# Performance work log

Hardware: AMD Instinct MI355X
Metric: run time of the kernel (lower is better)

The kernel has to match this reference:

```python
import jax, jax.numpy as jnp
import numpy as np

N_NODES = 50000
N_EDGES = 300000
N_CLUSTERS = 100
IN_C = 256
OUT_C = 256


def setup_inputs() -> dict:
    key = jax.random.key(0)
    k1, k2, k3, k4, k5, k6 = jax.random.split(key, 6)
    X = jax.random.normal(k1, (N_NODES, IN_C), dtype=jnp.float32)
    # Cluster-GCN style block partition: contiguous clusters of equal size
    assign = ((jnp.arange(N_NODES) * N_CLUSTERS) // N_NODES).astype(jnp.int32)
    bs = N_NODES // N_CLUSTERS  # block (cluster) size
    src = jax.random.randint(k2, (N_EDGES,), 0, N_NODES)
    intra_dst = (src // bs) * bs + jax.random.randint(k3, (N_EDGES,), 0, bs)
    rand_dst = jax.random.randint(k4, (N_EDGES,), 0, N_NODES)
    dst = jnp.where(jax.random.uniform(k5, (N_EDGES,)) < 0.9, intra_dst, rand_dst)
    full_ei = jnp.stack([src, dst]).astype(jnp.int32)
    W = (jax.random.normal(k6, (IN_C, OUT_C), dtype=jnp.float32) / np.sqrt(IN_C)).astype(jnp.float32)
    b = jnp.zeros((OUT_C,), dtype=jnp.float32)
    return {"X": X, "W": W, "b": b, "assign": assign, "full_ei": full_ei}


def reference(X, W, b, assign, full_ei):
    # Equivalent to the per-cluster loop: GCNConv (add_self_loops=True, symmetric
    # normalization) applied to the subgraph of intra-cluster edges; clusters
    # with zero internal edges are skipped (nodes keep original features).
    N = X.shape[0]
    src, dst = full_ei[0], full_ei[1]
    intra = (assign[src] == assign[dst]).astype(X.dtype)  # [E]
    # per-cluster-subgraph degree, including self loop
    deg = jnp.ones((N,), X.dtype).at[dst].add(intra)  # [N]
    dis = jax.lax.rsqrt(deg)
    xW = X @ W  # [N, out_c]
    w_e = intra * dis[src] * dis[dst]  # [E]
    agg = jax.ops.segment_sum(w_e[:, None] * xW[src], dst, num_segments=N)
    agg = agg + xW / deg[:, None]  # self-loop term: norm = 1/deg
    out = agg + b
    has_edge = jax.ops.segment_sum(intra, assign[src], num_segments=N_CLUSTERS) > 0
    return jnp.where(has_edge[assign][:, None], out, X)
```

## Files before the change

kernel.cpp:

```cpp
#include <hip/hip_runtime.h>
#include <hip/hip_bf16.h>

#define N_NODES 50000
#define N_EDGES 300000
#define N_CLUSTERS 100
#define CH 256
#define CAP 32

typedef __attribute__((ext_vector_type(8))) short short8;
typedef __attribute__((ext_vector_type(4))) float f32x4;

static __device__ inline unsigned short f2bf(float f) {
    unsigned int u = __float_as_uint(f);
    u += 0x7fffu + ((u >> 16) & 1u);
    return (unsigned short)(u >> 16);
}


__global__ void init_kernel(int* __restrict__ indeg, int* __restrict__ flags) {
    int i = blockIdx.x * blockDim.x + threadIdx.x;
    if (i < N_NODES) indeg[i] = 0;
    if (i < N_CLUSTERS) flags[i] = 0;
}

__global__ void scatter_kernel(const int* __restrict__ ei, const int* __restrict__ assign,
                               int* __restrict__ indeg, int* __restrict__ flags,
                               int* __restrict__ csr) {
    int e = blockIdx.x * blockDim.x + threadIdx.x;
    if (e >= N_EDGES) return;
    int s = ei[e], d = ei[N_EDGES + e];
    int cs = assign[s];
    if (cs == assign[d]) {
        int p = atomicAdd(&indeg[d], 1);
        if (p < CAP) csr[d * CAP + p] = s;
        flags[cs] = 1;
    }
}

__global__ void convw_kernel(const float* __restrict__ W, unsigned short* __restrict__ Wt) {
    int n = blockIdx.x, k = threadIdx.x;
    Wt[n * CH + k] = f2bf(W[k * CH + n]);
}


#define BM 64
#define ALDS 264

__global__ __launch_bounds__(256, 2) void gemm_bf16(const float* __restrict__ X,
                                                    const unsigned short* __restrict__ Wt,
                                                    unsigned short* __restrict__ xWb) {
    __shared__ unsigned short Xs[BM * ALDS];
    int tid = threadIdx.x;
    int row0 = blockIdx.x * BM;
    int wid = tid >> 6, lane = tid & 63;
    int wn = wid * 64;
    int l15 = lane & 15, quad = lane >> 4;

    short8 breg[4][8];
#pragma unroll
    for (int ni = 0; ni < 4; ++ni) {
        const unsigned short* p = Wt + (size_t)(wn + ni * 16 + l15) * CH + quad * 8;
#pragma unroll
        for (int c = 0; c < 8; ++c)
            breg[ni][c] = *reinterpret_cast<const short8*>(p + c * 32);
    }

    int srow = tid >> 2;
    int scol = (tid & 3) * 64;
    int garow = row0 + srow; if (garow >= N_NODES) garow = N_NODES - 1;
    const float* gA = X + (size_t)garow * CH + scol;
    unsigned short* lA = &Xs[srow * ALDS + scol];
#pragma unroll
    for (int j = 0; j < 16; j += 2) {
        float4 u = *reinterpret_cast<const float4*>(gA + j * 4);
        float4 v = *reinterpret_cast<const float4*>(gA + j * 4 + 4);
        ushort4 lo = { f2bf(u.x), f2bf(u.y), f2bf(u.z), f2bf(u.w) };
        ushort4 hi = { f2bf(v.x), f2bf(v.y), f2bf(v.z), f2bf(v.w) };
        uint4 packed;
        packed.x = (unsigned)lo.x | ((unsigned)lo.y << 16);
        packed.y = (unsigned)lo.z | ((unsigned)lo.w << 16);
        packed.z = (unsigned)hi.x | ((unsigned)hi.y << 16);
        packed.w = (unsigned)hi.z | ((unsigned)hi.w << 16);
        *reinterpret_cast<uint4*>(lA + j * 4) = packed;
    }
    __syncthreads();

    f32x4 acc[4][4] = {};
#pragma unroll
    for (int c = 0; c < 8; ++c) {
        short8 af[4];
#pragma unroll
        for (int mi = 0; mi < 4; ++mi)
            af[mi] = *reinterpret_cast<const short8*>(
                &Xs[(mi * 16 + l15) * ALDS + c * 32 + quad * 8]);
#pragma unroll
        for (int mi = 0; mi < 4; ++mi)
#pragma unroll
            for (int ni = 0; ni < 4; ++ni)
                acc[mi][ni] = __builtin_amdgcn_mfma_f32_16x16x32_bf16(
                    af[mi], breg[ni][c], acc[mi][ni], 0, 0, 0);
    }

#pragma unroll
    for (int mi = 0; mi < 4; ++mi)
#pragma unroll
        for (int r = 0; r < 4; ++r) {
            int grow = row0 + mi * 16 + quad * 4 + r;
            if (grow < N_NODES) {
                size_t rb = (size_t)grow * CH + wn + l15;
#pragma unroll
                for (int ni = 0; ni < 4; ++ni)
                    xWb[rb + ni * 16] = f2bf(acc[mi][ni][r]);
            }
        }
}


#define NBLK ((N_NODES + 3) / 4)
#define BLK_PER_XCD ((NBLK + 7) / 8)

static __device__ inline void bf4_fma(float w, uint2 v, float& ax, float& ay, float& az, float& aw) {
    ax += w * __uint_as_float(v.x << 16);
    ay += w * __uint_as_float(v.x & 0xffff0000u);
    az += w * __uint_as_float(v.y << 16);
    aw += w * __uint_as_float(v.y & 0xffff0000u);
}

__global__ __launch_bounds__(256) void gather_kernel(const unsigned short* __restrict__ xWb,
        const float* __restrict__ X, const float* __restrict__ b,
        const int* __restrict__ assign, const int* __restrict__ flags,
        const int* __restrict__ indeg, const int* __restrict__ csr,
        float* __restrict__ out) {
    int blk = (blockIdx.x & 7) * BLK_PER_XCD + (blockIdx.x >> 3);
    if (blk >= NBLK) return;
    int node = blk * 4 + (threadIdx.x >> 6);
    int lane = threadIdx.x & 63;
    if (node >= N_NODES) return;
    float4* out4 = reinterpret_cast<float4*>(out);
    size_t base4 = (size_t)node * 64 + lane;
    if (flags[assign[node]] == 0) {
        out4[base4] = reinterpret_cast<const float4*>(X)[base4];
        return;
    }
    int cnt_raw = indeg[node];
    int cnt = cnt_raw > CAP ? CAP : cnt_raw;
    float dn = rsqrtf(1.0f + (float)cnt_raw);

    int   s_l = 0;
    float w_l = 0.0f;
    if (lane < cnt) {
        s_l = csr[node * CAP + lane];
        w_l = rsqrtf(1.0f + (float)indeg[s_l]) * dn;
    }

    float selfw = dn * dn;
    uint2 sv = *reinterpret_cast<const uint2*>(xWb + (size_t)node * CH + lane * 4);
    float ax = 0, ay = 0, az = 0, aw = 0;
    bf4_fma(selfw, sv, ax, ay, az, aw);

    int cnt4 = (cnt + 3) & ~3;
    for (int i = 0; i < cnt4; i += 4) {
        int   s0 = __shfl(s_l, i),     s1 = __shfl(s_l, i + 1);
        int   s2 = __shfl(s_l, i + 2), s3 = __shfl(s_l, i + 3);
        float w0 = __shfl(w_l, i),     w1 = __shfl(w_l, i + 1);
        float w2 = __shfl(w_l, i + 2), w3 = __shfl(w_l, i + 3);
        uint2 v0 = *reinterpret_cast<const uint2*>(xWb + (size_t)s0 * CH + lane * 4);
        uint2 v1 = *reinterpret_cast<const uint2*>(xWb + (size_t)s1 * CH + lane * 4);
        uint2 v2 = *reinterpret_cast<const uint2*>(xWb + (size_t)s2 * CH + lane * 4);
        uint2 v3 = *reinterpret_cast<const uint2*>(xWb + (size_t)s3 * CH + lane * 4);
        bf4_fma(w0, v0, ax, ay, az, aw);
        bf4_fma(w1, v1, ax, ay, az, aw);
        bf4_fma(w2, v2, ax, ay, az, aw);
        bf4_fma(w3, v3, ax, ay, az, aw);
    }

    float4 bb = reinterpret_cast<const float4*>(b)[lane];
    float4 o = { ax + bb.x, ay + bb.y, az + bb.z, aw + bb.w };
    out4[base4] = o;
}


extern "C" void kernel_launch(void* const* d_in, const int* in_sizes, int n_in,
                              void* d_out, int out_size, void* d_ws, size_t ws_size,
                              hipStream_t stream) {
    const float* X      = (const float*)d_in[0];
    const float* W      = (const float*)d_in[1];
    const float* b      = (const float*)d_in[2];
    const int*   assign = (const int*)d_in[3];
    const int*   ei     = (const int*)d_in[4];
    float* out = (float*)d_out;

    char* ws = (char*)d_ws;
    size_t off = 0;
    auto alloc = [&](size_t bytes) -> void* {
        void* p = ws + off;
        off = (off + bytes + 255) & ~(size_t)255;
        return p;
    };
    unsigned short* xWb = (unsigned short*)alloc((size_t)N_NODES * CH * sizeof(unsigned short));
    unsigned short* Wt  = (unsigned short*)alloc((size_t)CH * CH * sizeof(unsigned short));
    int*   csr   = (int*)alloc((size_t)N_NODES * CAP * sizeof(int));
    int*   indeg = (int*)alloc(N_NODES * sizeof(int));
    int*   flags = (int*)alloc(N_CLUSTERS * sizeof(int));
    (void)ws_size; (void)n_in; (void)in_sizes; (void)out_size;

    init_kernel<<<(N_NODES + 255) / 256, 256, 0, stream>>>(indeg, flags);
    scatter_kernel<<<(N_EDGES + 255) / 256, 256, 0, stream>>>(ei, assign, indeg, flags, csr);
    convw_kernel<<<CH, CH, 0, stream>>>(W, Wt);
    gemm_bf16<<<(N_NODES + BM - 1) / BM, 256, 0, stream>>>(X, Wt, xWb);
    gather_kernel<<<BLK_PER_XCD * 8, 256, 0, stream>>>(xWb, X, b, assign, flags, indeg,
                                                       csr, out);
}
```

Measured before the change: 172.0 us.

## Widen gather to 16-byte loads, precompute inverse sqrt degree, merge prep kernels

The gather kernel now assigns 32 lanes per node, so each block handles 8 nodes and each lane loads 8 bf16 values (16 bytes) per neighbour instead of 4. The wave's shuffles are offset so each half-wave reads its own neighbour list. Inverse sqrt degrees are computed once per node inside the GEMM kernel and stored in a new buffer, so the gather reads a float instead of re-reading indeg and calling rsqrt for every neighbour. The weight transpose and zero-initialisation are merged into one prep kernel to save a launch, and the cluster flag is only written when it is still zero, which cuts redundant stores. The trade-off is an extra workspace buffer and a small dependency of the GEMM on indeg.

Result: faster. 167.5 us (-2.7%).

```diff
diff --git a/kernel.cpp b/kernel.cpp
--- a/kernel.cpp
+++ b/kernel.cpp
@@ -1,5 +1,4 @@
 #include <hip/hip_runtime.h>
-#include <hip/hip_bf16.h>
 
 #define N_NODES 50000
 #define N_EDGES 300000
@@ -16,11 +15,13 @@
     return (unsigned short)(u >> 16);
 }
 
-
-__global__ void init_kernel(int* __restrict__ indeg, int* __restrict__ flags) {
-    int i = blockIdx.x * blockDim.x + threadIdx.x;
+__global__ void prep_kernel(const float* __restrict__ W, unsigned short* __restrict__ Wt,
+                            int* __restrict__ indeg, int* __restrict__ flags) {
+    int i = blockIdx.x * 256 + threadIdx.x;
     if (i < N_NODES) indeg[i] = 0;
     if (i < N_CLUSTERS) flags[i] = 0;
+    int n = i >> 8, k = i & 255;
+    Wt[i] = f2bf(W[(size_t)k * CH + n]);
 }
 
 __global__ void scatter_kernel(const int* __restrict__ ei, const int* __restrict__ assign,
@@ -33,13 +34,8 @@
     if (cs == assign[d]) {
         int p = atomicAdd(&indeg[d], 1);
         if (p < CAP) csr[d * CAP + p] = s;
-        flags[cs] = 1;
-    }
-}
-
-__global__ void convw_kernel(const float* __restrict__ W, unsigned short* __restrict__ Wt) {
-    int n = blockIdx.x, k = threadIdx.x;
-    Wt[n * CH + k] = f2bf(W[k * CH + n]);
+        if (flags[cs] == 0) flags[cs] = 1;
+    }
 }
 
 
@@ -48,10 +44,18 @@
 
 __global__ __launch_bounds__(256, 2) void gemm_bf16(const float* __restrict__ X,
                                                     const unsigned short* __restrict__ Wt,
+                                                    const int* __restrict__ indeg,
+                                                    float* __restrict__ dis,
                                                     unsigned short* __restrict__ xWb) {
     __shared__ unsigned short Xs[BM * ALDS];
     int tid = threadIdx.x;
     int row0 = blockIdx.x * BM;
+
+    if (tid < 64) {
+        int r = row0 + tid;
+        if (r < N_NODES) dis[r] = rsqrtf(1.0f + (float)indeg[r]);
+    }
+
     int wid = tid >> 6, lane = tid & 63;
     int wn = wid * 64;
     int l15 = lane & 15, quad = lane >> 4;
@@ -116,67 +120,79 @@
 }
 
 
-#define NBLK ((N_NODES + 3) / 4)
-#define BLK_PER_XCD ((NBLK + 7) / 8)
-
-static __device__ inline void bf4_fma(float w, uint2 v, float& ax, float& ay, float& az, float& aw) {
-    ax += w * __uint_as_float(v.x << 16);
-    ay += w * __uint_as_float(v.x & 0xffff0000u);
-    az += w * __uint_as_float(v.y << 16);
-    aw += w * __uint_as_float(v.y & 0xffff0000u);
+#define NIDX 6250
+#define IDX_PER_XCD 782
+
+static __device__ inline void bf8_fma(float w, uint4 v, float* a) {
+    a[0] += w * __uint_as_float(v.x << 16);
+    a[1] += w * __uint_as_float(v.x & 0xffff0000u);
+    a[2] += w * __uint_as_float(v.y << 16);
+    a[3] += w * __uint_as_float(v.y & 0xffff0000u);
+    a[4] += w * __uint_as_float(v.z << 16);
+    a[5] += w * __uint_as_float(v.z & 0xffff0000u);
+    a[6] += w * __uint_as_float(v.w << 16);
+    a[7] += w * __uint_as_float(v.w & 0xffff0000u);
 }
 
 __global__ __launch_bounds__(256) void gather_kernel(const unsigned short* __restrict__ xWb,
         const float* __restrict__ X, const float* __restrict__ b,
-        const int* __restrict__ assign, const int* __restrict__ flags,
-        const int* __restrict__ indeg, const int* __restrict__ csr,
-        float* __restrict__ out) {
-    int blk = (blockIdx.x & 7) * BLK_PER_XCD + (blockIdx.x >> 3);
-    if (blk >= NBLK) return;
-    int node = blk * 4 + (threadIdx.x >> 6);
-    int lane = threadIdx.x & 63;
-    if (node >= N_NODES) return;
-    float4* out4 = reinterpret_cast<float4*>(out);
-    size_t base4 = (size_t)node * 64 + lane;
+        const float* __restrict__ dis, const int* __restrict__ assign,
+        const int* __restrict__ flags, const int* __restrict__ indeg,
+        const int* __restrict__ csr, float* __restrict__ out) {
+    int idx = (blockIdx.x & 7) * IDX_PER_XCD + (blockIdx.x >> 3);
+    if (idx >= NIDX) return;
+    int tid = threadIdx.x;
+    int grp = tid >> 5;
+    int gl  = tid & 31;
+    int node = idx * 8 + grp;
+    size_t rb = (size_t)node * CH + gl * 8;
+
     if (flags[assign[node]] == 0) {
-        out4[base4] = reinterpret_cast<const float4*>(X)[base4];
+        float4 u = *reinterpret_cast<const float4*>(X + rb);
+        float4 v = *reinterpret_cast<const float4*>(X + rb + 4);
+        *reinterpret_cast<float4*>(out + rb) = u;
+        *reinterpret_cast<float4*>(out + rb + 4) = v;
         return;
     }
+
     int cnt_raw = indeg[node];
     int cnt = cnt_raw > CAP ? CAP : cnt_raw;
-    float dn = rsqrtf(1.0f + (float)cnt_raw);
+    float dn = dis[node];
 
     int   s_l = 0;
     float w_l = 0.0f;
-    if (lane < cnt) {
-        s_l = csr[node * CAP + lane];
-        w_l = rsqrtf(1.0f + (float)indeg[s_l]) * dn;
-    }
-
-    float selfw = dn * dn;
-    uint2 sv = *reinterpret_cast<const uint2*>(xWb + (size_t)node * CH + lane * 4);
-    float ax = 0, ay = 0, az = 0, aw = 0;
-    bf4_fma(selfw, sv, ax, ay, az, aw);
-
+    if (gl < cnt) {
+        s_l = csr[node * CAP + gl];
+        w_l = dis[s_l] * dn;
+    }
+
+    float a[8] = {};
+    uint4 sv = *reinterpret_cast<const uint4*>(xWb + rb);
+    bf8_fma(dn * dn, sv, a);
+
+    int gbase = ((tid >> 5) & 1) << 5;
     int cnt4 = (cnt + 3) & ~3;
-    for (int i = 0; i < cnt4; i += 4) {
-        int   s0 = __shfl(s_l, i),     s1 = __shfl(s_l, i + 1);
-        int   s2 = __shfl(s_l, i + 2), s3 = __shfl(s_l, i + 3);
-        float w0 = __shfl(w_l, i),     w1 = __shfl(w_l, i + 1);
-        float w2 = __shfl(w_l, i + 2), w3 = __shfl(w_l, i + 3);
-        uint2 v0 = *reinterpret_cast<const uint2*>(xWb + (size_t)s0 * CH + lane * 4);
-        uint2 v1 = *reinterpret_cast<const uint2*>(xWb + (size_t)s1 * CH + lane * 4);
-        uint2 v2 = *reinterpret_cast<const uint2*>(xWb + (size_t)s2 * CH + lane * 4);
-        uint2 v3 = *reinterpret_cast<const uint2*>(xWb + (size_t)s3 * CH + lane * 4);
-        bf4_fma(w0, v0, ax, ay, az, aw);
-        bf4_fma(w1, v1, ax, ay, az, aw);
-        bf4_fma(w2, v2, ax, ay, az, aw);
-        bf4_fma(w3, v3, ax, ay, az, aw);
-    }
-
-    float4 bb = reinterpret_cast<const float4*>(b)[lane];
-    float4 o = { ax + bb.x, ay + bb.y, az + bb.z, aw + bb.w };
-    out4[base4] = o;
+    for (int k = 0; k < cnt4; k += 4) {
+        int   s0 = __shfl(s_l, gbase + k),     s1 = __shfl(s_l, gbase + k + 1);
+        int   s2 = __shfl(s_l, gbase + k + 2), s3 = __shfl(s_l, gbase + k + 3);
+        float w0 = __shfl(w_l, gbase + k),     w1 = __shfl(w_l, gbase + k + 1);
+        float w2 = __shfl(w_l, gbase + k + 2), w3 = __shfl(w_l, gbase + k + 3);
+        uint4 v0 = *reinterpret_cast<const uint4*>(xWb + (size_t)s0 * CH + gl * 8);
+        uint4 v1 = *reinterpret_cast<const uint4*>(xWb + (size_t)s1 * CH + gl * 8);
+        uint4 v2 = *reinterpret_cast<const uint4*>(xWb + (size_t)s2 * CH + gl * 8);
+        uint4 v3 = *reinterpret_cast<const uint4*>(xWb + (size_t)s3 * CH + gl * 8);
+        bf8_fma(w0, v0, a);
+        bf8_fma(w1, v1, a);
+        bf8_fma(w2, v2, a);
+        bf8_fma(w3, v3, a);
+    }
+
+    float4 b0 = *reinterpret_cast<const float4*>(b + gl * 8);
+    float4 b1 = *reinterpret_cast<const float4*>(b + gl * 8 + 4);
+    float4 o0 = { a[0] + b0.x, a[1] + b0.y, a[2] + b0.z, a[3] + b0.w };
+    float4 o1 = { a[4] + b1.x, a[5] + b1.y, a[6] + b1.z, a[7] + b1.w };
+    *reinterpret_cast<float4*>(out + rb) = o0;
+    *reinterpret_cast<float4*>(out + rb + 4) = o1;
 }
 
 
@@ -201,13 +217,13 @@
     unsigned short* Wt  = (unsigned short*)alloc((size_t)CH * CH * sizeof(unsigned short));
     int*   csr   = (int*)alloc((size_t)N_NODES * CAP * sizeof(int));
     int*   indeg = (int*)alloc(N_NODES * sizeof(int));
+    float* dis   = (float*)alloc(N_NODES * sizeof(float));
     int*   flags = (int*)alloc(N_CLUSTERS * sizeof(int));
     (void)ws_size; (void)n_in; (void)in_sizes; (void)out_size;
 
-    init_kernel<<<(N_NODES + 255) / 256, 256, 0, stream>>>(indeg, flags);
+    prep_kernel<<<256, 256, 0, stream>>>(W, Wt, indeg, flags);
     scatter_kernel<<<(N_EDGES + 255) / 256, 256, 0, stream>>>(ei, assign, indeg, flags, csr);
-    convw_kernel<<<CH, CH, 0, stream>>>(W, Wt);
-    gemm_bf16<<<(N_NODES + BM - 1) / BM, 256, 0, stream>>>(X, Wt, xWb);
-    gather_kernel<<<BLK_PER_XCD * 8, 256, 0, stream>>>(xWb, X, b, assign, flags, indeg,
-                                                       csr, out);
-}
+    gemm_bf16<<<(N_NODES + BM - 1) / BM, 256, 0, stream>>>(X, Wt, indeg, dis, xWb);
+    gather_kernel<<<IDX_PER_XCD * 8, 256, 0, stream>>>(xWb, X, b, dis, assign, flags,
+                                                       indeg, csr, out);
+}
```
